# Optimization experiments

Hardware: AMD Instinct MI355X
Metric: run time of the kernel (lower is better)

The kernel has to match this reference:

```python
import jax, jax.numpy as jnp
import numpy as np

B, T, DIM, DIM_EPS, H = 4, 1024, 2048, 2048, 16
HD = DIM // H        # 128, value head dim
HDE = DIM_EPS // H   # 128, q/k head dim


def setup_inputs() -> dict:
    key = jax.random.key(0)
    ks = jax.random.split(key, 6)
    s = 0.02
    # rotary frequencies as in llama-style precompute (theta=10000)
    inv_freq = 1.0 / (10000.0 ** (np.arange(0, HDE, 2, dtype=np.float32) / HDE))
    t = np.arange(T, dtype=np.float32)
    ang = np.outer(t, inv_freq)  # (T, HDE//2)
    return {
        "v": jax.random.normal(ks[0], (B, T, DIM), jnp.float32),
        "x_eps": jax.random.normal(ks[1], (B, T, DIM_EPS), jnp.float32),
        "freqs_cos": jnp.asarray(np.cos(ang)),
        "freqs_sin": jnp.asarray(np.sin(ang)),
        "W_eps_attn": jax.random.normal(ks[2], (DIM_EPS, 2 * DIM_EPS), jnp.float32) * s,
        "W_attn": jax.random.normal(ks[3], (DIM, DIM), jnp.float32) * s,
        "W_proj": jax.random.normal(ks[4], (DIM, DIM), jnp.float32) * s,
        "W_eps_proj": jax.random.normal(ks[5], (DIM_EPS, DIM_EPS), jnp.float32) * s,
    }


def _rope(x, cos, sin):
    # x: (B, T, H, HDE) -> complex-multiply by freqs_cis of shape (T, HDE//2)
    xr = x.reshape(*x.shape[:-1], -1, 2)
    x_re, x_im = xr[..., 0], xr[..., 1]
    c = cos[None, :, None, :]  # (1, T, 1, HDE//2)
    s = sin[None, :, None, :]
    o_re = x_re * c - x_im * s
    o_im = x_re * s + x_im * c
    return jnp.stack([o_re, o_im], axis=-1).reshape(x.shape)


def reference(v, x_eps, freqs_cos, freqs_sin, W_eps_attn, W_attn, W_proj, W_eps_proj):
    Bn, Tn, C = v.shape
    qk = x_eps @ W_eps_attn            # (B, T, 2*DIM_EPS)
    q, k = jnp.split(qk, 2, axis=-1)
    vp = v @ W_attn                    # (B, T, DIM)
    q = _rope(q.reshape(Bn, Tn, H, HDE), freqs_cos, freqs_sin)
    k = _rope(k.reshape(Bn, Tn, H, HDE), freqs_cos, freqs_sin)
    q = q.transpose(0, 2, 1, 3)        # (B, H, T, HDE)
    k = k.transpose(0, 2, 1, 3)
    vh = vp.reshape(Bn, Tn, H, HD).transpose(0, 2, 1, 3)
    scale = 1.0 / jnp.sqrt(jnp.asarray(HDE, q.dtype))
    scores = jnp.einsum("bhqd,bhkd->bhqk", q, k) * scale
    causal = jnp.tril(jnp.ones((Tn, Tn), bool))
    scores = jnp.where(causal[None, None], scores, jnp.finfo(scores.dtype).min)
    att = jax.nn.softmax(scores, axis=-1)
    y = jnp.einsum("bhqk,bhkd->bhqd", att, vh)
    y = y.transpose(0, 2, 1, 3).reshape(Bn, Tn, C)
    v_out = y @ W_proj
    x_eps_out = x_eps @ W_eps_proj
    return (v_out, x_eps_out)
```

## Files before the change

kernel.cpp:

```cpp
#include <hip/hip_runtime.h>
#include <stdint.h>

typedef __attribute__((ext_vector_type(8))) short  short8;
typedef __attribute__((ext_vector_type(4))) float  f32x4;
typedef __attribute__((ext_vector_type(4))) float  float4v;
typedef __attribute__((ext_vector_type(4))) unsigned short ushort4v;

#define DEV __device__ __forceinline__

DEV unsigned short f2bf(float f) {
    union { float f; unsigned int u; } x; x.f = f;
    unsigned int u = x.u;
    unsigned int r = (u + 0x7fffu + ((u >> 16) & 1u)) >> 16;
    return (unsigned short)r;
}
DEV float bf2f(unsigned short b) {
    union { unsigned int u; float f; } x; x.u = ((unsigned int)b) << 16;
    return x.f;
}

DEV void gll16(const void* g, void* l) {
    __builtin_amdgcn_global_load_lds(
        (const __attribute__((address_space(1))) void*)g,
        (__attribute__((address_space(3))) void*)l, 16, 0, 0);
}

#define MROWS 4096
#define KDIM  2048
#define NQK   4096

__global__ void cast_f32_bf16(const float* __restrict__ in,
                              unsigned short* __restrict__ out, int n4) {
    int i = blockIdx.x * blockDim.x + threadIdx.x;
    if (i < n4) {
        float4v f = ((const float4v*)in)[i];
        ushort4v o;
        o[0] = f2bf(f[0]); o[1] = f2bf(f[1]); o[2] = f2bf(f[2]); o[3] = f2bf(f[3]);
        ((ushort4v*)out)[i] = o;
    }
}

__global__ void transpose_cast(const float* __restrict__ W,
                               unsigned short* __restrict__ Wt, int K, int N) {
    __shared__ float tile[32][33];
    int tx = threadIdx.x, ty = threadIdx.y;
    int n0 = blockIdx.x * 32, k0 = blockIdx.y * 32;
#pragma unroll
    for (int j = 0; j < 32; j += 8)
        tile[ty + j][tx] = W[(size_t)(k0 + ty + j) * N + n0 + tx];
    __syncthreads();
#pragma unroll
    for (int j = 0; j < 32; j += 8)
        Wt[(size_t)(n0 + ty + j) * K + k0 + tx] = f2bf(tile[tx][ty + j]);
}

__global__ void transpose_v(const unsigned short* __restrict__ vp,
                            unsigned short* __restrict__ vpT) {
    __shared__ unsigned short tile[32][34];
    int tx = threadIdx.x, ty = threadIdx.y;
    int R0 = blockIdx.y * 32;
    int c0 = blockIdx.x * 32;
    int bh = R0 >> 7, d0 = R0 & 127;
    int b = bh >> 4, h = bh & 15;
#pragma unroll
    for (int j = 0; j < 32; j += 8)
        tile[ty + j][tx] = vp[(size_t)(b * 1024 + c0 + ty + j) * 2048 + h * 128 + d0 + tx];
    __syncthreads();
#pragma unroll
    for (int j = 0; j < 32; j += 8)
        vpT[(size_t)(R0 + ty + j) * 1024 + c0 + tx] = tile[tx][ty + j];
}

__global__ __launch_bounds__(512, 2) void gemm256(
    const unsigned short* __restrict__ A0g, const unsigned short* __restrict__ B0g,
    float* __restrict__ Cf0, unsigned short* __restrict__ Ch0,
    int N0, int tx0, int nb0, int outbf0,
    const unsigned short* __restrict__ A1g, const unsigned short* __restrict__ B1g,
    float* __restrict__ Cf1, unsigned short* __restrict__ Ch1,
    int N1, int tx1, int outbf1, int K) {

    __shared__ __align__(16) char lds[131072];

    int blk = blockIdx.x;
    const unsigned short* Ag; const unsigned short* Bg;
    float* Cf; unsigned short* Ch; int N, tx, outbf;
    if (blk < nb0) { Ag = A0g; Bg = B0g; Cf = Cf0; Ch = Ch0; N = N0; tx = tx0; outbf = outbf0; }
    else { blk -= nb0; Ag = A1g; Bg = B1g; Cf = Cf1; Ch = Ch1; N = N1; tx = tx1; outbf = outbf1; }
    const int bx = blk % tx, by = blk / tx;

    const int tid = threadIdx.x;
    const int lane = tid & 63;
    const int w  = tid >> 6;
    const int lr = lane & 15, lk = lane >> 4;
    const int wm = w >> 2, wn = w & 3;
    const int cswz16 = (lk ^ ((lr >> 3) << 1)) * 16;

    const unsigned short* Arow = Ag + (size_t)(by * 256) * K;
    const unsigned short* Brow = Bg + (size_t)(bx * 256) * K;

    auto STAGE = [&](const unsigned short* srcHalf, int k0, char* ldsHalf) {
        int row  = tid >> 2;
        int clog = (tid & 3) ^ (((tid >> 5) & 1) << 1);
        const unsigned short* g = srcHalf + (size_t)row * K + k0 + clog * 8;
        gll16(g,      ldsHalf + tid * 16);
        gll16(g + 32, ldsHalf + 8192 + tid * 16);
    };

    f32x4 acc[8][4];
#pragma unroll
    for (int m = 0; m < 8; ++m)
#pragma unroll
        for (int n = 0; n < 4; ++n) acc[m][n] = (f32x4){0.f, 0.f, 0.f, 0.f};

    const int NT = K >> 6;
    char* buf0 = lds;
    char* buf1 = lds + 65536;

    STAGE(Brow,                   0, buf0 + 32768);
    STAGE(Brow + (size_t)128 * K, 0, buf0 + 32768 + 16384);
    STAGE(Arow,                   0, buf0);
    STAGE(Arow + (size_t)128 * K, 0, buf0 + 16384);
    STAGE(Brow,                  64, buf1 + 32768);
    STAGE(Brow + (size_t)128 * K, 64, buf1 + 32768 + 16384);
    asm volatile("s_waitcnt vmcnt(4)" ::: "memory");
    __builtin_amdgcn_s_barrier();

#define GPHASE(MF0, MF1, STAGE_STMT, TAIL_STMT)                                   \
    {                                                                             \
        short8 afr0[2], afr1[2];                                                  \
        afr0[0] = *(const short8*)(aBase +        (MF0 * 16 + lr) * 64 + cswz16); \
        afr0[1] = *(const short8*)(aBase + 8192 + (MF0 * 16 + lr) * 64 + cswz16); \
        afr1[0] = *(const short8*)(aBase +        (MF1 * 16 + lr) * 64 + cswz16); \
        afr1[1] = *(const short8*)(aBase + 8192 + (MF1 * 16 + lr) * 64 + cswz16); \
        STAGE_STMT;                                                               \
        __builtin_amdgcn_sched_barrier(0);                                        \
        __builtin_amdgcn_s_barrier();                                             \
        asm volatile("s_waitcnt lgkmcnt(0)" ::: "memory");                        \
        __builtin_amdgcn_sched_barrier(0);                                        \
        __builtin_amdgcn_s_setprio(1);                                            \
        _Pragma("unroll")                                                         \
        for (int ks = 0; ks < 2; ++ks)                                            \
            _Pragma("unroll")                                                     \
            for (int nf = 0; nf < 4; ++nf) {                                      \
                acc[MF0][nf] = __builtin_amdgcn_mfma_f32_16x16x32_bf16(           \
                    afr0[ks], bfr[nf][ks], acc[MF0][nf], 0, 0, 0);                \
                acc[MF1][nf] = __builtin_amdgcn_mfma_f32_16x16x32_bf16(           \
                    afr1[ks], bfr[nf][ks], acc[MF1][nf], 0, 0, 0);                \
            }                                                                     \
        __builtin_amdgcn_s_setprio(0);                                            \
        __builtin_amdgcn_sched_barrier(0);                                        \
        TAIL_STMT;                                                                \
        __builtin_amdgcn_s_barrier();                                             \
    }

    for (int u = 0; u < NT; ++u) {
        char* bufC = (u & 1) ? buf1 : buf0;
        char* bufN = (u & 1) ? buf0 : buf1;
        const char* aBase = bufC + wm * 16384;
        const char* bBase = bufC + 32768 + (wn >> 1) * 16384;
        const int bRow0 = (wn & 1) * 64;
        const bool stA = (u + 1 < NT), stB = (u + 2 < NT);

        short8 bfr[4][2];
#pragma unroll
        for (int nf = 0; nf < 4; ++nf) {
            bfr[nf][0] = *(const short8*)(bBase +        (bRow0 + nf * 16 + lr) * 64 + cswz16);
            bfr[nf][1] = *(const short8*)(bBase + 8192 + (bRow0 + nf * 16 + lr) * 64 + cswz16);
        }

        GPHASE(0, 1, { if (stA) STAGE(Arow,                   (u + 1) * 64, bufN); }, {})
        GPHASE(2, 3, { if (stA) STAGE(Arow + (size_t)128 * K, (u + 1) * 64, bufN + 16384); }, {})
        GPHASE(4, 5, { if (stB) STAGE(Brow,                   (u + 2) * 64, bufC + 32768); }, {})
        GPHASE(6, 7, { if (stB) STAGE(Brow + (size_t)128 * K, (u + 2) * 64, bufC + 32768 + 16384); },
               { if (stB) { asm volatile("s_waitcnt vmcnt(4)" ::: "memory"); }
                 else     { asm volatile("s_waitcnt vmcnt(0)" ::: "memory"); } })
    }
#undef GPHASE

    if (outbf) {
#pragma unroll
        for (int mf = 0; mf < 8; ++mf)
#pragma unroll
            for (int nf = 0; nf < 4; ++nf)
#pragma unroll
                for (int r = 0; r < 4; ++r) {
                    int row = by * 256 + wm * 128 + mf * 16 + lk * 4 + r;
                    int col = bx * 256 + wn * 64 + nf * 16 + lr;
                    Ch[(size_t)row * N + col] = f2bf(acc[mf][nf][r]);
                }
    } else {
#pragma unroll
        for (int mf = 0; mf < 8; ++mf)
#pragma unroll
            for (int nf = 0; nf < 4; ++nf)
#pragma unroll
                for (int r = 0; r < 4; ++r) {
                    int row = by * 256 + wm * 128 + mf * 16 + lk * 4 + r;
                    int col = bx * 256 + wn * 64 + nf * 16 + lr;
                    Cf[(size_t)row * N + col] = acc[mf][nf][r];
                }
    }
}

__global__ void rope_kernel(unsigned short* __restrict__ qk,
                            const float* __restrict__ fcos,
                            const float* __restrict__ fsin) {
    int idx  = blockIdx.x * 256 + threadIdx.x;
    int row  = idx >> 9;
    int g    = idx & 511;
    int t    = row & 1023;
    int half = g >> 8;
    int hp   = g & 255;
    int h    = hp >> 4;
    int ig   = hp & 15;
    int col  = half * 2048 + h * 128 + ig * 8;
    size_t off = (size_t)row * 4096 + col;

    short8 v = *(short8*)(qk + off);
    int i0 = ig * 4;
    float4v c = *(const float4v*)(fcos + t * 64 + i0);
    float4v s = *(const float4v*)(fsin + t * 64 + i0);
    short8 o;
#pragma unroll
    for (int p = 0; p < 4; ++p) {
        float re = bf2f((unsigned short)v[2 * p]);
        float im = bf2f((unsigned short)v[2 * p + 1]);
        o[2 * p]     = (short)f2bf(re * c[p] - im * s[p]);
        o[2 * p + 1] = (short)f2bf(re * s[p] + im * c[p]);
    }
    *(short8*)(qk + off) = o;
}

__global__ __launch_bounds__(256) void attn_kernel(
    const unsigned short* __restrict__ qk,
    const unsigned short* __restrict__ vpT,
    unsigned short* __restrict__ y) {

    const int bh = blockIdx.x;
    const int qt = 7 - (int)blockIdx.y;
    const int b = bh >> 4, h = bh & 15;
    const int qb0 = qt * 128;

    __shared__ __align__(16) unsigned short Kt[64 * 128];
    __shared__ __align__(16) unsigned short Vt[128 * 64];
    __shared__ __align__(16) unsigned short Pl[4 * 32 * 72];

    const int tid = threadIdx.x, w = tid >> 6, lane = tid & 63;
    const int lr = lane & 15, lk = lane >> 4;

    const unsigned short* Qb = qk + (size_t)(b * 1024) * 4096 + h * 128;
    const unsigned short* Kb = Qb + 2048;
    const unsigned short* Vg = vpT + (size_t)bh * 128 * 1024;
    unsigned short* Pw = &Pl[w * 32 * 72];

    short8 qf[2][4];
#pragma unroll
    for (int m = 0; m < 2; ++m) {
        const unsigned short* qrow = Qb + (size_t)(qb0 + w * 32 + m * 16 + lr) * 4096;
#pragma unroll
        for (int db = 0; db < 4; ++db)
            qf[m][db] = *(const short8*)(qrow + db * 32 + lk * 8);
    }

    f32x4 acc[2][8];
#pragma unroll
    for (int m = 0; m < 2; ++m)
#pragma unroll
        for (int n = 0; n < 8; ++n) acc[m][n] = (f32x4){0.f, 0.f, 0.f, 0.f};
    float m_i[2][4], l_i[2][4];
#pragma unroll
    for (int m = 0; m < 2; ++m)
#pragma unroll
        for (int r = 0; r < 4; ++r) { m_i[m][r] = -1e30f; l_i[m][r] = 0.f; }

    const int nkt = 2 * qt + 2;
    for (int kt = 0; kt < nkt; ++kt) {
#pragma unroll
        for (int c = 0; c < 4; ++c) {
            int base = w * 4096 + c * 1024;
            int row  = (base >> 8) + (lane >> 4);
            int colB = (lane & 15) * 16;
            int scol = colB ^ ((row & 7) << 4);
            gll16(Kb + (size_t)(kt * 64 + row) * 4096 + (scol >> 1),
                  (char*)Kt + base);
        }
#pragma unroll
        for (int c = 0; c < 4; ++c) {
            int base = w * 4096 + c * 1024;
            int d    = (base >> 7) + (lane >> 3);
            int colB = (lane & 7) * 16;
            int scol = colB ^ ((d & 7) << 4);
            gll16(Vg + (size_t)d * 1024 + kt * 64 + (scol >> 1),
                  (char*)Vt + base);
        }
        __syncthreads();

        f32x4 s[2][4];
#pragma unroll
        for (int m = 0; m < 2; ++m)
#pragma unroll
            for (int n = 0; n < 4; ++n) s[m][n] = (f32x4){0.f, 0.f, 0.f, 0.f};
#pragma unroll
        for (int db = 0; db < 4; ++db)
#pragma unroll
            for (int n = 0; n < 4; ++n) {
                int krow = n * 16 + lr;
                int cb = (db * 64 + lk * 16) ^ ((krow & 7) << 4);
                short8 kf = *(const short8*)((const char*)Kt + krow * 256 + cb);
                s[0][n] = __builtin_amdgcn_mfma_f32_16x16x32_bf16(qf[0][db], kf, s[0][n], 0, 0, 0);
                s[1][n] = __builtin_amdgcn_mfma_f32_16x16x32_bf16(qf[1][db], kf, s[1][n], 0, 0, 0);
            }

        const float sc = 0.08838834764831845f;
        const bool diag = (kt >= 2 * qt);
#pragma unroll
        for (int m = 0; m < 2; ++m)
#pragma unroll
            for (int n = 0; n < 4; ++n)
#pragma unroll
                for (int r = 0; r < 4; ++r) {
                    float v = s[m][n][r] * sc;
                    if (diag) {
                        int q   = qb0 + w * 32 + m * 16 + lk * 4 + r;
                        int key = kt * 64 + n * 16 + lr;
                        if (key > q) v = -1e30f;
                    }
                    s[m][n][r] = v;
                }

#pragma unroll
        for (int m = 0; m < 2; ++m) {
            float pm[4];
#pragma unroll
            for (int r = 0; r < 4; ++r)
                pm[r] = fmaxf(fmaxf(s[m][0][r], s[m][1][r]), fmaxf(s[m][2][r], s[m][3][r]));
#pragma unroll
            for (int o = 1; o < 16; o <<= 1)
#pragma unroll
                for (int r = 0; r < 4; ++r)
                    pm[r] = fmaxf(pm[r], __shfl_xor(pm[r], o, 16));

            float resc[4], rs[4];
#pragma unroll
            for (int r = 0; r < 4; ++r) {
                float mn = fmaxf(m_i[m][r], pm[r]);
                resc[r] = __expf(m_i[m][r] - mn);
                m_i[m][r] = mn;
                rs[r] = 0.f;
            }
#pragma unroll
            for (int n = 0; n < 4; ++n)
#pragma unroll
                for (int r = 0; r < 4; ++r) {
                    float p = __expf(s[m][n][r] - m_i[m][r]);
                    s[m][n][r] = p;
                    rs[r] += p;
                }
#pragma unroll
            for (int o = 1; o < 16; o <<= 1)
#pragma unroll
                for (int r = 0; r < 4; ++r)
                    rs[r] += __shfl_xor(rs[r], o, 16);
#pragma unroll
            for (int r = 0; r < 4; ++r)
                l_i[m][r] = l_i[m][r] * resc[r] + rs[r];
#pragma unroll
            for (int n = 0; n < 8; ++n)
#pragma unroll
                for (int r = 0; r < 4; ++r)
                    acc[m][n][r] *= resc[r];

#pragma unroll
            for (int n = 0; n < 4; ++n)
#pragma unroll
                for (int r = 0; r < 4; ++r)
                    Pw[(m * 16 + lk * 4 + r) * 72 + n * 16 + lr] = f2bf(s[m][n][r]);
        }

#pragma unroll
        for (int ks = 0; ks < 2; ++ks) {
            short8 pf0 = *(const short8*)&Pw[(lr) * 72 + ks * 32 + lk * 8];
            short8 pf1 = *(const short8*)&Pw[(16 + lr) * 72 + ks * 32 + lk * 8];
#pragma unroll
            for (int n8 = 0; n8 < 8; ++n8) {
                int d  = n8 * 16 + lr;
                int cb = (ks * 64 + lk * 16) ^ ((d & 7) << 4);
                short8 vf = *(const short8*)((const char*)Vt + d * 128 + cb);
                acc[0][n8] = __builtin_amdgcn_mfma_f32_16x16x32_bf16(pf0, vf, acc[0][n8], 0, 0, 0);
                acc[1][n8] = __builtin_amdgcn_mfma_f32_16x16x32_bf16(pf1, vf, acc[1][n8], 0, 0, 0);
            }
        }
        __syncthreads();
    }

    unsigned short* yb = y + (size_t)(b * 1024) * 2048 + h * 128;
#pragma unroll
    for (int m = 0; m < 2; ++m)
#pragma unroll
        for (int n8 = 0; n8 < 8; ++n8)
#pragma unroll
            for (int r = 0; r < 4; ++r) {
                int t = qb0 + w * 32 + m * 16 + lk * 4 + r;
                int d = n8 * 16 + lr;
                yb[(size_t)t * 2048 + d] = f2bf(acc[m][n8][r] / l_i[m][r]);
            }
}

extern "C" void kernel_launch(void* const* d_in, const int* in_sizes, int n_in,
                              void* d_out, int out_size, void* d_ws, size_t ws_size,
                              hipStream_t stream) {
    const float* v_in  = (const float*)d_in[0];
    const float* xeps  = (const float*)d_in[1];
    const float* fcos  = (const float*)d_in[2];
    const float* fsin  = (const float*)d_in[3];
    const float* Wea   = (const float*)d_in[4];
    const float* Wa    = (const float*)d_in[5];
    const float* Wp    = (const float*)d_in[6];
    const float* Wep   = (const float*)d_in[7];
    float* out = (float*)d_out;

    char* ws = (char*)d_ws;
    unsigned short* xe16 = (unsigned short*)ws;  ws += (size_t)MROWS * KDIM * 2;
    unsigned short* v16  = (unsigned short*)ws;  ws += (size_t)MROWS * KDIM * 2;
    unsigned short* WeaT = (unsigned short*)ws;  ws += (size_t)NQK * KDIM * 2;
    unsigned short* WaT  = (unsigned short*)ws;  ws += (size_t)KDIM * KDIM * 2;
    unsigned short* WpT  = (unsigned short*)ws;  ws += (size_t)KDIM * KDIM * 2;
    unsigned short* WepT = (unsigned short*)ws;  ws += (size_t)KDIM * KDIM * 2;
    unsigned short* qk16 = (unsigned short*)ws;  ws += (size_t)MROWS * NQK * 2;
    unsigned short* vp16 = (unsigned short*)ws;  ws += (size_t)MROWS * KDIM * 2;
    unsigned short* y16  = (unsigned short*)ws;  ws += (size_t)MROWS * KDIM * 2;
    unsigned short* vpT  = v16;

    cast_f32_bf16<<<8192, 256, 0, stream>>>(xeps, xe16, MROWS * KDIM / 4);
    cast_f32_bf16<<<8192, 256, 0, stream>>>(v_in, v16,  MROWS * KDIM / 4);

    transpose_cast<<<dim3(NQK / 32, KDIM / 32), dim3(32, 8), 0, stream>>>(Wea, WeaT, KDIM, NQK);
    transpose_cast<<<dim3(KDIM / 32, KDIM / 32), dim3(32, 8), 0, stream>>>(Wa,  WaT,  KDIM, KDIM);
    transpose_cast<<<dim3(KDIM / 32, KDIM / 32), dim3(32, 8), 0, stream>>>(Wp,  WpT,  KDIM, KDIM);
    transpose_cast<<<dim3(KDIM / 32, KDIM / 32), dim3(32, 8), 0, stream>>>(Wep, WepT, KDIM, KDIM);

    gemm256<<<256, 512, 0, stream>>>(
        xe16, WeaT, nullptr, qk16, NQK, 16, 256, 1,
        xe16, WeaT, nullptr, qk16, NQK, 16, 1, KDIM);

    rope_kernel<<<8192, 256, 0, stream>>>(qk16, fcos, fsin);

    gemm256<<<256, 512, 0, stream>>>(
        v16,  WaT,  nullptr, vp16, KDIM, 8, 128, 1,
        xe16, WepT, out + (size_t)MROWS * KDIM, nullptr, KDIM, 8, 0, KDIM);

    transpose_v<<<dim3(1024 / 32, 8192 / 32), dim3(32, 8), 0, stream>>>(vp16, vpT);

    attn_kernel<<<dim3(64, 8), 256, 0, stream>>>(qk16, vpT, y16);

    gemm256<<<128, 512, 0, stream>>>(
        y16, WpT, out, nullptr, KDIM, 8, 128, 0,
        y16, WpT, out, nullptr, KDIM, 8, 0, KDIM);
}
```

Before: 327.4 us.

## Double-buffer A fragments across GEMM phases and remap blocks for XCD locality

Restructures the GEMM inner loop so A-fragment LDS reads for the next phase are issued before the MFMAs of the current phase, using two register sets and partial lgkmcnt waits. This hides LDS read latency behind matrix math. Also remaps block indices so consecutive tiles land on the same XCD, which is meant to improve L2 reuse. The extra fragment registers raise register pressure, and the remap assumes the block count divides by 8.

```diff
diff --git a/kernel.cpp b/kernel.cpp
--- a/kernel.cpp
+++ b/kernel.cpp
@@ -83,9 +83,10 @@
 
     int blk = blockIdx.x;
     const unsigned short* Ag; const unsigned short* Bg;
-    float* Cf; unsigned short* Ch; int N, tx, outbf;
-    if (blk < nb0) { Ag = A0g; Bg = B0g; Cf = Cf0; Ch = Ch0; N = N0; tx = tx0; outbf = outbf0; }
-    else { blk -= nb0; Ag = A1g; Bg = B1g; Cf = Cf1; Ch = Ch1; N = N1; tx = tx1; outbf = outbf1; }
+    float* Cf; unsigned short* Ch; int N, tx, outbf, nwg;
+    if (blk < nb0) { Ag = A0g; Bg = B0g; Cf = Cf0; Ch = Ch0; N = N0; tx = tx0; outbf = outbf0; nwg = nb0; }
+    else { blk -= nb0; Ag = A1g; Bg = B1g; Cf = Cf1; Ch = Ch1; N = N1; tx = tx1; outbf = outbf1; nwg = gridDim.x - nb0; }
+    { int cpx = nwg >> 3; blk = (blk & 7) * cpx + (blk >> 3); }
     const int bx = blk % tx, by = blk / tx;
 
     const int tid = threadIdx.x;
@@ -125,33 +126,27 @@
     asm volatile("s_waitcnt vmcnt(4)" ::: "memory");
     __builtin_amdgcn_s_barrier();
 
-#define GPHASE(MF0, MF1, STAGE_STMT, TAIL_STMT)                                   \
-    {                                                                             \
-        short8 afr0[2], afr1[2];                                                  \
-        afr0[0] = *(const short8*)(aBase +        (MF0 * 16 + lr) * 64 + cswz16); \
-        afr0[1] = *(const short8*)(aBase + 8192 + (MF0 * 16 + lr) * 64 + cswz16); \
-        afr1[0] = *(const short8*)(aBase +        (MF1 * 16 + lr) * 64 + cswz16); \
-        afr1[1] = *(const short8*)(aBase + 8192 + (MF1 * 16 + lr) * 64 + cswz16); \
-        STAGE_STMT;                                                               \
-        __builtin_amdgcn_sched_barrier(0);                                        \
-        __builtin_amdgcn_s_barrier();                                             \
-        asm volatile("s_waitcnt lgkmcnt(0)" ::: "memory");                        \
-        __builtin_amdgcn_sched_barrier(0);                                        \
-        __builtin_amdgcn_s_setprio(1);                                            \
-        _Pragma("unroll")                                                         \
-        for (int ks = 0; ks < 2; ++ks)                                            \
-            _Pragma("unroll")                                                     \
-            for (int nf = 0; nf < 4; ++nf) {                                      \
-                acc[MF0][nf] = __builtin_amdgcn_mfma_f32_16x16x32_bf16(           \
-                    afr0[ks], bfr[nf][ks], acc[MF0][nf], 0, 0, 0);                \
-                acc[MF1][nf] = __builtin_amdgcn_mfma_f32_16x16x32_bf16(           \
-                    afr1[ks], bfr[nf][ks], acc[MF1][nf], 0, 0, 0);                \
-            }                                                                     \
-        __builtin_amdgcn_s_setprio(0);                                            \
-        __builtin_amdgcn_sched_barrier(0);                                        \
-        TAIL_STMT;                                                                \
-        __builtin_amdgcn_s_barrier();                                             \
-    }
+#define MFMA_BF(a, b, c) __builtin_amdgcn_mfma_f32_16x16x32_bf16(a, b, c, 0, 0, 0)
+
+#define LDAFR(DST, P)                                                                \
+    DST[0] = *(const short8*)(aBase +        ((P) * 32 +      lr) * 64 + cswz16);    \
+    DST[1] = *(const short8*)(aBase + 8192 + ((P) * 32 +      lr) * 64 + cswz16);    \
+    DST[2] = *(const short8*)(aBase +        ((P) * 32 + 16 + lr) * 64 + cswz16);    \
+    DST[3] = *(const short8*)(aBase + 8192 + ((P) * 32 + 16 + lr) * 64 + cswz16);
+
+#define MFMA16(P, R)                                                       \
+    __builtin_amdgcn_s_setprio(1);                                         \
+    _Pragma("unroll")                                                      \
+    for (int nf = 0; nf < 4; ++nf) {                                       \
+        acc[2*(P)][nf]   = MFMA_BF(R[0], BC[nf][0], acc[2*(P)][nf]);       \
+        acc[2*(P)+1][nf] = MFMA_BF(R[2], BC[nf][0], acc[2*(P)+1][nf]);     \
+    }                                                                      \
+    _Pragma("unroll")                                                      \
+    for (int nf = 0; nf < 4; ++nf) {                                       \
+        acc[2*(P)][nf]   = MFMA_BF(R[1], BC[nf][1], acc[2*(P)][nf]);       \
+        acc[2*(P)+1][nf] = MFMA_BF(R[3], BC[nf][1], acc[2*(P)+1][nf]);     \
+    }                                                                      \
+    __builtin_amdgcn_s_setprio(0);
 
     for (int u = 0; u < NT; ++u) {
         char* bufC = (u & 1) ? buf1 : buf0;
@@ -161,21 +156,45 @@
         const int bRow0 = (wn & 1) * 64;
         const bool stA = (u + 1 < NT), stB = (u + 2 < NT);
 
-        short8 bfr[4][2];
+        short8 BC[4][2];
 #pragma unroll
         for (int nf = 0; nf < 4; ++nf) {
-            bfr[nf][0] = *(const short8*)(bBase +        (bRow0 + nf * 16 + lr) * 64 + cswz16);
-            bfr[nf][1] = *(const short8*)(bBase + 8192 + (bRow0 + nf * 16 + lr) * 64 + cswz16);
+            BC[nf][0] = *(const short8*)(bBase +        (bRow0 + nf * 16 + lr) * 64 + cswz16);
+            BC[nf][1] = *(const short8*)(bBase + 8192 + (bRow0 + nf * 16 + lr) * 64 + cswz16);
         }
-
-        GPHASE(0, 1, { if (stA) STAGE(Arow,                   (u + 1) * 64, bufN); }, {})
-        GPHASE(2, 3, { if (stA) STAGE(Arow + (size_t)128 * K, (u + 1) * 64, bufN + 16384); }, {})
-        GPHASE(4, 5, { if (stB) STAGE(Brow,                   (u + 2) * 64, bufC + 32768); }, {})
-        GPHASE(6, 7, { if (stB) STAGE(Brow + (size_t)128 * K, (u + 2) * 64, bufC + 32768 + 16384); },
-               { if (stB) { asm volatile("s_waitcnt vmcnt(4)" ::: "memory"); }
-                 else     { asm volatile("s_waitcnt vmcnt(0)" ::: "memory"); } })
-    }
-#undef GPHASE
+        short8 Ra[4], Rb[4];
+        LDAFR(Ra, 0)
+        LDAFR(Rb, 1)
+        if (stA) STAGE(Arow, (u + 1) * 64, bufN);
+        asm volatile("s_waitcnt lgkmcnt(4)" ::: "memory");
+        __builtin_amdgcn_s_barrier();
+        MFMA16(0, Ra)
+        __builtin_amdgcn_s_barrier();
+
+        LDAFR(Ra, 2)
+        if (stA) STAGE(Arow + (size_t)128 * K, (u + 1) * 64, bufN + 16384);
+        asm volatile("s_waitcnt lgkmcnt(4)" ::: "memory");
+        __builtin_amdgcn_s_barrier();
+        MFMA16(1, Rb)
+        __builtin_amdgcn_s_barrier();
+
+        LDAFR(Rb, 3)
+        if (stB) STAGE(Brow, (u + 2) * 64, bufC + 32768);
+        asm volatile("s_waitcnt lgkmcnt(4)" ::: "memory");
+        __builtin_amdgcn_s_barrier();
+        MFMA16(2, Ra)
+        __builtin_amdgcn_s_barrier();
+
+        if (stB) STAGE(Brow + (size_t)128 * K, (u + 2) * 64, bufC + 32768 + 16384);
+        asm volatile("s_waitcnt lgkmcnt(0)" ::: "memory");
+        __builtin_amdgcn_s_barrier();
+        MFMA16(3, Rb)
+        if (stB) { asm volatile("s_waitcnt vmcnt(4)" ::: "memory"); }
+        else     { asm volatile("s_waitcnt vmcnt(0)" ::: "memory"); }
+        __builtin_amdgcn_s_barrier();
+    }
+#undef LDAFR
+#undef MFMA16
 
     if (outbf) {
 #pragma unroll
```

After: 330.9 us. About the same (+1.1%).
